# Optimization experiments

Hardware: AMD Instinct MI355X
Metric: run time of the kernel (lower is better)

Reference implementation:

```python
import jax, jax.numpy as jnp
import numpy as np

N_NODES = 1024
IN_FEATURES = 512
N_HEADS = 4
N_HIDDEN = 32  # out_features (128) // n_heads (4)
NEG_SLOPE = 0.2


def setup_inputs() -> dict:
    key = jax.random.key(0)
    k1, k2, k3, k4, k5 = jax.random.split(key, 5)
    h = jax.random.normal(k1, (N_NODES, IN_FEATURES), dtype=jnp.float32)
    adj_mat = jax.random.randint(k2, (N_NODES, N_NODES, 1), 0, 2, dtype=jnp.int32)
    s = 1.0 / np.sqrt(IN_FEATURES)
    W_l = jax.random.uniform(k3, (IN_FEATURES, N_HEADS * N_HIDDEN), jnp.float32, -s, s)
    W_r = jax.random.uniform(k4, (IN_FEATURES, N_HEADS * N_HIDDEN), jnp.float32, -s, s)
    sa = 1.0 / np.sqrt(N_HIDDEN)
    attn_w = jax.random.uniform(k5, (N_HIDDEN,), jnp.float32, -sa, sa)
    return {"h": h, "adj_mat": adj_mat, "W_l": W_l, "W_r": W_r, "attn_w": attn_w}


def reference(h, adj_mat, W_l, W_r, attn_w):
    # GraphAttentionV2Layer forward (eval mode: dropout = identity)
    n = h.shape[0]
    g_l = (h @ W_l).reshape(n, N_HEADS, N_HIDDEN)  # source-side (j)
    g_r = (h @ W_r).reshape(n, N_HEADS, N_HIDDEN)  # dest-side (i)
    # g_sum[i, j, h, f] = g_l[j] + g_r[i]  (repeat / repeat_interleave semantics)
    g_sum = g_l[None, :, :, :] + g_r[:, None, :, :]  # [N, N, H, hid]
    act = jnp.where(g_sum >= 0, g_sum, NEG_SLOPE * g_sum)
    e = jnp.einsum('ijhf,f->ijh', act, attn_w)  # [N, N, H]
    mask = (adj_mat == 0)  # broadcasts [N, N, 1] -> [N, N, H]
    e = jnp.where(mask, -jnp.inf, e)
    a = jax.nn.softmax(e, axis=1)  # softmax over neighbors j
    h_prime = jnp.einsum('ijh,jhf->ihf', a, g_r)  # note: aggregates g_r, per source
    h_prime = h_prime.reshape(n, N_HEADS * N_HIDDEN)  # is_concat=True
    # not output layer -> ELU activation (output dropout is identity in eval)
    out = jnp.where(h_prime > 0, h_prime, jnp.expm1(h_prime))
    return out
```

## Files before the change

### kernel.cpp

```cpp
#include <hip/hip_runtime.h>
#include <math.h>

#define N_NODES 1024
#define IN_F 512
#define N_HEADS 4
#define N_HID 32
#define OUT_F 128
#define GF 256
#define NEG_SLOPE 0.2f

__global__ __launch_bounds__(256, 2) void gat_gemm(
    const float* __restrict__ hmat, const float* __restrict__ Wl,
    const float* __restrict__ Wr, const int* __restrict__ adj,
    float* __restrict__ gpart, unsigned long long* __restrict__ bits)
{
  const int b = blockIdx.x;
  const int kc = b & 7, ct = (b >> 3) & 3, it = b >> 5;
  const int i0 = it * 64, k0 = kc * 64, cb0 = ct * 64;
  const float* __restrict__ W = (cb0 < 128) ? (Wl + cb0) : (Wr + (cb0 - 128));

  __shared__ float As[16][68];
  __shared__ float Bs[16][64];

  const int tx = threadIdx.x & 15, ty = threadIdx.x >> 4;
  const int ar = threadIdx.x >> 2, ak = (threadIdx.x & 3) * 4;
  const int bk = threadIdx.x >> 4, bc = (threadIdx.x & 15) * 4;

  float4 acc0 = {0.f, 0.f, 0.f, 0.f}, acc1 = acc0, acc2 = acc0, acc3 = acc0;

  float4 av = *(const float4*)(hmat + (size_t)(i0 + ar) * IN_F + k0 + ak);
  float4 bv = *(const float4*)(W + (size_t)(k0 + bk) * OUT_F + bc);

  for (int t = 0; t < 64; t += 16) {
    __syncthreads();
    As[ak + 0][ar] = av.x; As[ak + 1][ar] = av.y;
    As[ak + 2][ar] = av.z; As[ak + 3][ar] = av.w;
    *(float4*)&Bs[bk][bc] = bv;
    __syncthreads();
    if (t < 48) {
      av = *(const float4*)(hmat + (size_t)(i0 + ar) * IN_F + k0 + t + 16 + ak);
      bv = *(const float4*)(W + (size_t)(k0 + t + 16 + bk) * OUT_F + bc);
    }
#pragma unroll
    for (int k = 0; k < 16; ++k) {
      const float4 a  = *(const float4*)&As[k][ty * 4];
      const float4 bb = *(const float4*)&Bs[k][tx * 4];
      acc0.x = fmaf(a.x, bb.x, acc0.x); acc0.y = fmaf(a.x, bb.y, acc0.y);
      acc0.z = fmaf(a.x, bb.z, acc0.z); acc0.w = fmaf(a.x, bb.w, acc0.w);
      acc1.x = fmaf(a.y, bb.x, acc1.x); acc1.y = fmaf(a.y, bb.y, acc1.y);
      acc1.z = fmaf(a.y, bb.z, acc1.z); acc1.w = fmaf(a.y, bb.w, acc1.w);
      acc2.x = fmaf(a.z, bb.x, acc2.x); acc2.y = fmaf(a.z, bb.y, acc2.y);
      acc2.z = fmaf(a.z, bb.z, acc2.z); acc2.w = fmaf(a.z, bb.w, acc2.w);
      acc3.x = fmaf(a.w, bb.x, acc3.x); acc3.y = fmaf(a.w, bb.y, acc3.y);
      acc3.z = fmaf(a.w, bb.z, acc3.z); acc3.w = fmaf(a.w, bb.w, acc3.w);
    }
  }
  const size_t rbase = (size_t)kc * N_NODES + i0 + ty * 4;
  const int cc = cb0 + tx * 4;
  *(float4*)(gpart + (rbase + 0) * GF + cc) = acc0;
  *(float4*)(gpart + (rbase + 1) * GF + cc) = acc1;
  *(float4*)(gpart + (rbase + 2) * GF + cc) = acc2;
  *(float4*)(gpart + (rbase + 3) * GF + cc) = acc3;

#pragma unroll
  for (int r = 0; r < 2; ++r) {
    const int i = b * 2 + r;
#pragma unroll
    for (int q = 0; q < 4; ++q) {
      const int j = q * 256 + threadIdx.x;
      const unsigned long long m =
          __ballot(adj[(size_t)i * N_NODES + j] != 0);
      if ((threadIdx.x & 63) == 0) bits[i * 16 + (j >> 6)] = m;
    }
  }
}

__global__ __launch_bounds__(256) void gat_reduceWab(
    const float* __restrict__ gpart, const float* __restrict__ attn_w,
    float* __restrict__ g, float* __restrict__ abuf, float* __restrict__ bbuf)
{
  const int tid = threadIdx.x;
  const int l = tid & 63, r = tid >> 6;
  const int row = blockIdx.x * 4 + r;
  const size_t o = (size_t)row * GF + l * 4;
  float4 s = *(const float4*)(gpart + o);
#pragma unroll
  for (int c = 1; c < 8; ++c) {
    const float4 v = *(const float4*)(gpart + (size_t)c * (N_NODES * GF) + o);
    s.x += v.x; s.y += v.y; s.z += v.z; s.w += v.w;
  }
  *(float4*)(g + o) = s;
  const float4 a4 = *(const float4*)(attn_w + (l & 7) * 4);
  float d = 0.6f * (s.x * a4.x + s.y * a4.y + s.z * a4.z + s.w * a4.w);
  d += __shfl_xor(d, 1);
  d += __shfl_xor(d, 2);
  d += __shfl_xor(d, 4);
  if ((l & 7) == 0) {
    const int hq = l >> 3;
    if (hq < 4) abuf[hq * N_NODES + row] = d;
    else        bbuf[(hq - 4) * N_NODES + row] = d;
  }
}

__global__ __launch_bounds__(256, 2) void gat_fused(
    const float* __restrict__ g, const float* __restrict__ attn_w,
    const float* __restrict__ abuf, const float* __restrict__ bbuf,
    const unsigned long long* __restrict__ bits,
    float* __restrict__ num_part, float* __restrict__ den_part)
{
  __shared__ float gj[32][256];
  __shared__ float ps[32][4][36];
  __shared__ float as_[4][32];

  const int b = blockIdx.x;
  const int jc = b & 15, it = b >> 4;
  const int i0 = it * 32, j0 = jc * 64;
  const int t = threadIdx.x;

  const int hh = t >> 6, half = (t >> 5) & 1, il = t & 31;
  const int i = i0 + il;
  const int fb1 = hh * N_HID + half * 16;

  const int ig = t >> 5, h2 = (t >> 3) & 3, fg = t & 7;

  const int wv = t >> 6, ln = t & 63;

  float4 gri[4], c2[4], num[4];
#pragma unroll
  for (int q = 0; q < 4; ++q) {
    gri[q] = *(const float4*)(g + (size_t)i * GF + 128 + fb1 + q * 4);
    const float4 a4 = *(const float4*)(attn_w + half * 16 + q * 4);
    c2[q] = make_float4(0.4f * a4.x, 0.4f * a4.y, 0.4f * a4.z, 0.4f * a4.w);
    num[q] = make_float4(0.f, 0.f, 0.f, 0.f);
  }
  const float beta = bbuf[hh * N_NODES + i];
  const unsigned long long bm = bits[(size_t)i * 16 + jc];
  float den_t = 0.f;

  for (int ts = 0; ts < 2; ++ts) {
    __syncthreads();
#pragma unroll
    for (int k = 0; k < 8; ++k) {
      const int r = wv * 8 + k;
      *(float4*)&gj[r][ln * 4] =
          *(const float4*)(g + (size_t)(j0 + ts * 32 + r) * GF + ln * 4);
    }
    if (t < 128)
      as_[t >> 5][t & 31] =
          abuf[(t >> 5) * N_NODES + j0 + ts * 32 + (t & 31)];
    __syncthreads();

    const unsigned int w32 = (unsigned int)(bm >> (ts * 32));
#pragma unroll 4
    for (int j = 0; j < 32; ++j) {
      float part = 0.f;
#pragma unroll
      for (int q = 0; q < 4; ++q) {
        const float4 gl = *(const float4*)&gj[j][fb1 + q * 4];
        float s;
        s = gl.x + gri[q].x; part = fmaf(c2[q].x, __builtin_fabsf(s), part);
        s = gl.y + gri[q].y; part = fmaf(c2[q].y, __builtin_fabsf(s), part);
        s = gl.z + gri[q].z; part = fmaf(c2[q].z, __builtin_fabsf(s), part);
        s = gl.w + gri[q].w; part = fmaf(c2[q].w, __builtin_fabsf(s), part);
      }
      const float full = part + __shfl_xor(part, 32);
      const float e = full + as_[hh][j] + beta;
      const float p = ((w32 >> j) & 1u) ? __expf(e) : 0.f;
      if (half == 0) ps[j][hh][il] = p;
      den_t += p;
    }
    __syncthreads();

#pragma unroll 4
    for (int j = 0; j < 32; ++j) {
      const float4 pv = *(const float4*)&ps[j][h2][ig * 4];
      const float4 gv = *(const float4*)&gj[j][128 + h2 * 32 + fg * 4];
      num[0].x = fmaf(pv.x, gv.x, num[0].x);
      num[0].y = fmaf(pv.x, gv.y, num[0].y);
      num[0].z = fmaf(pv.x, gv.z, num[0].z);
      num[0].w = fmaf(pv.x, gv.w, num[0].w);
      num[1].x = fmaf(pv.y, gv.x, num[1].x);
      num[1].y = fmaf(pv.y, gv.y, num[1].y);
      num[1].z = fmaf(pv.y, gv.z, num[1].z);
      num[1].w = fmaf(pv.y, gv.w, num[1].w);
      num[2].x = fmaf(pv.z, gv.x, num[2].x);
      num[2].y = fmaf(pv.z, gv.y, num[2].y);
      num[2].z = fmaf(pv.z, gv.z, num[2].z);
      num[2].w = fmaf(pv.z, gv.w, num[2].w);
      num[3].x = fmaf(pv.w, gv.x, num[3].x);
      num[3].y = fmaf(pv.w, gv.y, num[3].y);
      num[3].z = fmaf(pv.w, gv.z, num[3].z);
      num[3].w = fmaf(pv.w, gv.w, num[3].w);
    }
  }

  if (half == 0)
    den_part[((size_t)jc * N_HEADS + hh) * N_NODES + i] = den_t;
  float* np = num_part + ((size_t)jc * N_NODES + i0 + ig * 4) * OUT_F +
              h2 * N_HID + fg * 4;
#pragma unroll
  for (int ii = 0; ii < 4; ++ii) {
    const float4 v = num[ii];
    *(float4*)(np + (size_t)ii * OUT_F) = v;
  }
}

__global__ __launch_bounds__(256) void gat_fin(
    const float* __restrict__ num_part, const float* __restrict__ den_part,
    float* __restrict__ outp)
{
  const int e4 = blockIdx.x * 256 + threadIdx.x;
  const int flat = e4 * 4;
  const int i = flat >> 7, hh = (flat & 127) >> 5;
  float4 s = {0.f, 0.f, 0.f, 0.f};
  float d = 0.f;
#pragma unroll
  for (int c = 0; c < 16; ++c) {
    const float4 v = *(const float4*)(num_part + (size_t)c * (N_NODES * OUT_F) + flat);
    s.x += v.x; s.y += v.y; s.z += v.z; s.w += v.w;
    d += den_part[((size_t)c * N_HEADS + hh) * N_NODES + i];
  }
  const float inv = 1.0f / d;
  float4 o;
  o.x = s.x * inv; o.y = s.y * inv; o.z = s.z * inv; o.w = s.w * inv;
  o.x = o.x > 0.f ? o.x : expm1f(o.x);
  o.y = o.y > 0.f ? o.y : expm1f(o.y);
  o.z = o.z > 0.f ? o.z : expm1f(o.z);
  o.w = o.w > 0.f ? o.w : expm1f(o.w);
  *(float4*)(outp + flat) = o;
}

extern "C" void kernel_launch(void* const* d_in, const int* in_sizes, int n_in,
                              void* d_out, int out_size, void* d_ws, size_t ws_size,
                              hipStream_t stream) {
  const float* hmat  = (const float*)d_in[0];
  const int*   adj   = (const int*)d_in[1];
  const float* Wl    = (const float*)d_in[2];
  const float* Wr    = (const float*)d_in[3];
  const float* attnw = (const float*)d_in[4];
  float* outp = (float*)d_out;

  char* ws = (char*)d_ws;
  float* gpart = (float*)(ws);
  float* g     = (float*)(ws + (8u << 20));
  float* abuf  = (float*)(ws + (9u << 20));
  float* bbuf  = (float*)(ws + (9u << 20) + (64u << 10));
  unsigned long long* bits =
      (unsigned long long*)(ws + (9u << 20) + (128u << 10));
  float* denp  = (float*)(ws + (9u << 20) + (256u << 10));
  float* nump  = (float*)(ws + (10u << 20));

  gat_gemm<<<512, 256, 0, stream>>>(hmat, Wl, Wr, adj, gpart, bits);
  gat_reduceWab<<<256, 256, 0, stream>>>(gpart, attnw, g, abuf, bbuf);
  gat_fused<<<512, 256, 0, stream>>>(g, attnw, abuf, bbuf, bits, nump, denp);
  gat_fin<<<128, 256, 0, stream>>>(nump, denp, outp);
}
```

Before: 101.5 us.

## Process two destination nodes per thread in fused attention kernel

Each thread in the fused attention kernel now handles two destination rows instead of one, so the i-tile grows from 32 to 64 and the grid is halved. Every gj value loaded from shared memory is reused for two score computations and two aggregation rows, which cuts LDS traffic and the repeated source-tile loads per output. The cost is more registers (8 float4 accumulators plus two gri sets), which may reduce occupancy, and only 256 blocks to spread across the CUs.

```diff
diff --git a/kernel.cpp b/kernel.cpp
--- a/kernel.cpp
+++ b/kernel.cpp
@@ -109,33 +109,37 @@
     float* __restrict__ num_part, float* __restrict__ den_part)
 {
   __shared__ float gj[32][256];
-  __shared__ float ps[32][4][36];
+  __shared__ float ps[32][4][68];
   __shared__ float as_[4][32];
 
   const int b = blockIdx.x;
   const int jc = b & 15, it = b >> 4;
-  const int i0 = it * 32, j0 = jc * 64;
+  const int i0 = it * 64, j0 = jc * 64;
   const int t = threadIdx.x;
 
-  const int hh = t >> 6, half = (t >> 5) & 1, il = t & 31;
-  const int i = i0 + il;
+  const int hh = t >> 6, half = (t >> 5) & 1, ilp = t & 31;
+  const int ia = i0 + ilp * 2;
   const int fb1 = hh * N_HID + half * 16;
 
   const int ig = t >> 5, h2 = (t >> 3) & 3, fg = t & 7;
 
   const int wv = t >> 6, ln = t & 63;
 
-  float4 gri[4], c2[4], num[4];
+  float4 gri0[4], gri1[4], c2[4], num[8];
 #pragma unroll
   for (int q = 0; q < 4; ++q) {
-    gri[q] = *(const float4*)(g + (size_t)i * GF + 128 + fb1 + q * 4);
+    gri0[q] = *(const float4*)(g + (size_t)(ia + 0) * GF + 128 + fb1 + q * 4);
+    gri1[q] = *(const float4*)(g + (size_t)(ia + 1) * GF + 128 + fb1 + q * 4);
     const float4 a4 = *(const float4*)(attn_w + half * 16 + q * 4);
     c2[q] = make_float4(0.4f * a4.x, 0.4f * a4.y, 0.4f * a4.z, 0.4f * a4.w);
-    num[q] = make_float4(0.f, 0.f, 0.f, 0.f);
-  }
-  const float beta = bbuf[hh * N_NODES + i];
-  const unsigned long long bm = bits[(size_t)i * 16 + jc];
-  float den_t = 0.f;
+  }
+#pragma unroll
+  for (int q = 0; q < 8; ++q) num[q] = make_float4(0.f, 0.f, 0.f, 0.f);
+  const float beta0 = bbuf[hh * N_NODES + ia + 0];
+  const float beta1 = bbuf[hh * N_NODES + ia + 1];
+  const unsigned long long bm0 = bits[(size_t)(ia + 0) * 16 + jc];
+  const unsigned long long bm1 = bits[(size_t)(ia + 1) * 16 + jc];
+  float den0 = 0.f, den1 = 0.f;
 
   for (int ts = 0; ts < 2; ++ts) {
     __syncthreads();
@@ -150,59 +154,83 @@
           abuf[(t >> 5) * N_NODES + j0 + ts * 32 + (t & 31)];
     __syncthreads();
 
-    const unsigned int w32 = (unsigned int)(bm >> (ts * 32));
-#pragma unroll 4
+    const unsigned int w0 = (unsigned int)(bm0 >> (ts * 32));
+    const unsigned int w1 = (unsigned int)(bm1 >> (ts * 32));
+#pragma unroll 2
     for (int j = 0; j < 32; ++j) {
-      float part = 0.f;
+      float p0 = 0.f, p1 = 0.f;
 #pragma unroll
       for (int q = 0; q < 4; ++q) {
         const float4 gl = *(const float4*)&gj[j][fb1 + q * 4];
         float s;
-        s = gl.x + gri[q].x; part = fmaf(c2[q].x, __builtin_fabsf(s), part);
-        s = gl.y + gri[q].y; part = fmaf(c2[q].y, __builtin_fabsf(s), part);
-        s = gl.z + gri[q].z; part = fmaf(c2[q].z, __builtin_fabsf(s), part);
-        s = gl.w + gri[q].w; part = fmaf(c2[q].w, __builtin_fabsf(s), part);
+        s = gl.x + gri0[q].x; p0 = fmaf(c2[q].x, __builtin_fabsf(s), p0);
+        s = gl.y + gri0[q].y; p0 = fmaf(c2[q].y, __builtin_fabsf(s), p0);
+        s = gl.z + gri0[q].z; p0 = fmaf(c2[q].z, __builtin_fabsf(s), p0);
+        s = gl.w + gri0[q].w; p0 = fmaf(c2[q].w, __builtin_fabsf(s), p0);
+        s = gl.x + gri1[q].x; p1 = fmaf(c2[q].x, __builtin_fabsf(s), p1);
+        s = gl.y + gri1[q].y; p1 = fmaf(c2[q].y, __builtin_fabsf(s), p1);
+        s = gl.z + gri1[q].z; p1 = fmaf(c2[q].z, __builtin_fabsf(s), p1);
+        s = gl.w + gri1[q].w; p1 = fmaf(c2[q].w, __builtin_fabsf(s), p1);
       }
-      const float full = part + __shfl_xor(part, 32);
-      const float e = full + as_[hh][j] + beta;
-      const float p = ((w32 >> j) & 1u) ? __expf(e) : 0.f;
-      if (half == 0) ps[j][hh][il] = p;
-      den_t += p;
+      const float f0 = p0 + __shfl_xor(p0, 32);
+      const float f1 = p1 + __shfl_xor(p1, 32);
+      const float aj = as_[hh][j];
+      float e0 = ((w0 >> j) & 1u) ? __expf(f0 + aj + beta0) : 0.f;
+      float e1 = ((w1 >> j) & 1u) ? __expf(f1 + aj + beta1) : 0.f;
+      den0 += e0; den1 += e1;
+      if (half == 0) *(float2*)&ps[j][hh][ilp * 2] = make_float2(e0, e1);
     }
     __syncthreads();
 
 #pragma unroll 4
     for (int j = 0; j < 32; ++j) {
-      const float4 pv = *(const float4*)&ps[j][h2][ig * 4];
+      const float4 pv0 = *(const float4*)&ps[j][h2][ig * 8];
+      const float4 pv1 = *(const float4*)&ps[j][h2][ig * 8 + 4];
       const float4 gv = *(const float4*)&gj[j][128 + h2 * 32 + fg * 4];
-      num[0].x = fmaf(pv.x, gv.x, num[0].x);
-      num[0].y = fmaf(pv.x, gv.y, num[0].y);
-      num[0].z = fmaf(pv.x, gv.z, num[0].z);
-      num[0].w = fmaf(pv.x, gv.w, num[0].w);
-      num[1].x = fmaf(pv.y, gv.x, num[1].x);
-      num[1].y = fmaf(pv.y, gv.y, num[1].y);
-      num[1].z = fmaf(pv.y, gv.z, num[1].z);
-      num[1].w = fmaf(pv.y, gv.w, num[1].w);
-      num[2].x = fmaf(pv.z, gv.x, num[2].x);
-      num[2].y = fmaf(pv.z, gv.y, num[2].y);
-      num[2].z = fmaf(pv.z, gv.z, num[2].z);
-      num[2].w = fmaf(pv.z, gv.w, num[2].w);
-      num[3].x = fmaf(pv.w, gv.x, num[3].x);
-      num[3].y = fmaf(pv.w, gv.y, num[3].y);
-      num[3].z = fmaf(pv.w, gv.z, num[3].z);
-      num[3].w = fmaf(pv.w, gv.w, num[3].w);
-    }
-  }
-
-  if (half == 0)
-    den_part[((size_t)jc * N_HEADS + hh) * N_NODES + i] = den_t;
-  float* np = num_part + ((size_t)jc * N_NODES + i0 + ig * 4) * OUT_F +
+      num[0].x = fmaf(pv0.x, gv.x, num[0].x);
+      num[0].y = fmaf(pv0.x, gv.y, num[0].y);
+      num[0].z = fmaf(pv0.x, gv.z, num[0].z);
+      num[0].w = fmaf(pv0.x, gv.w, num[0].w);
+      num[1].x = fmaf(pv0.y, gv.x, num[1].x);
+      num[1].y = fmaf(pv0.y, gv.y, num[1].y);
+      num[1].z = fmaf(pv0.y, gv.z, num[1].z);
+      num[1].w = fmaf(pv0.y, gv.w, num[1].w);
+      num[2].x = fmaf(pv0.z, gv.x, num[2].x);
+      num[2].y = fmaf(pv0.z, gv.y, num[2].y);
+      num[2].z = fmaf(pv0.z, gv.z, num[2].z);
+      num[2].w = fmaf(pv0.z, gv.w, num[2].w);
+      num[3].x = fmaf(pv0.w, gv.x, num[3].x);
+      num[3].y = fmaf(pv0.w, gv.y, num[3].y);
+      num[3].z = fmaf(pv0.w, gv.z, num[3].z);
+      num[3].w = fmaf(pv0.w, gv.w, num[3].w);
+      num[4].x = fmaf(pv1.x, gv.x, num[4].x);
+      num[4].y = fmaf(pv1.x, gv.y, num[4].y);
+      num[4].z = fmaf(pv1.x, gv.z, num[4].z);
+      num[4].w = fmaf(pv1.x, gv.w, num[4].w);
+      num[5].x = fmaf(pv1.y, gv.x, num[5].x);
+      num[5].y = fmaf(pv1.y, gv.y, num[5].y);
+      num[5].z = fmaf(pv1.y, gv.z, num[5].z);
+      num[5].w = fmaf(pv1.y, gv.w, num[5].w);
+      num[6].x = fmaf(pv1.z, gv.x, num[6].x);
+      num[6].y = fmaf(pv1.z, gv.y, num[6].y);
+      num[6].z = fmaf(pv1.z, gv.z, num[6].z);
+      num[6].w = fmaf(pv1.z, gv.w, num[6].w);
+      num[7].x = fmaf(pv1.w, gv.x, num[7].x);
+      num[7].y = fmaf(pv1.w, gv.y, num[7].y);
+      num[7].z = fmaf(pv1.w, gv.z, num[7].z);
+      num[7].w = fmaf(pv1.w, gv.w, num[7].w);
+    }
+  }
+
+  if (half == 0) {
+    den_part[((size_t)jc * N_HEADS + hh) * N_NODES + ia + 0] = den0;
+    den_part[((size_t)jc * N_HEADS + hh) * N_NODES + ia + 1] = den1;
+  }
+  float* np = num_part + ((size_t)jc * N_NODES + i0 + ig * 8) * OUT_F +
               h2 * N_HID + fg * 4;
 #pragma unroll
-  for (int ii = 0; ii < 4; ++ii) {
-    const float4 v = num[ii];
-    *(float4*)(np + (size_t)ii * OUT_F) = v;
-  }
+  for (int ii = 0; ii < 8; ++ii)
+    *(float4*)(np + (size_t)ii * OUT_F) = num[ii];
 }
 
 __global__ __launch_bounds__(256) void gat_fin(
@@ -252,6 +280,6 @@
 
   gat_gemm<<<512, 256, 0, stream>>>(hmat, Wl, Wr, adj, gpart, bits);
   gat_reduceWab<<<256, 256, 0, stream>>>(gpart, attnw, g, abuf, bbuf);
-  gat_fused<<<512, 256, 0, stream>>>(g, attnw, abuf, bbuf, bits, nump, denp);
+  gat_fused<<<256, 256, 0, stream>>>(g, attnw, abuf, bbuf, bits, nump, denp);
   gat_fin<<<128, 256, 0, stream>>>(nump, denp, outp);
 }
```

Measured after the change: 105.6 us. 1.04x slower.
